# Performance work log

Hardware: AMD Instinct MI355X
Metric: run time of the kernel (lower is better)

Reference implementation:

```python
import jax, jax.numpy as jnp
import numpy as np

N = 50000        # nodes
E = 1_600_000    # edges
F = 32           # in/out channels
T = 4            # towers
FT = F // T      # per-tower channels = 8
ED = 16          # edge_dim
L = 5            # num PNA layers


def setup_inputs() -> dict:
    key = jax.random.key(0)
    ks = jax.random.split(key, 11)
    s = 0.2  # weight scale
    return {
        "x": jax.random.normal(ks[0], (N, F), jnp.float32),
        "edge_index": jax.random.randint(ks[1], (2, E), 0, N, dtype=jnp.int32),
        "edge_attr": jax.random.normal(ks[2], (E, ED), jnp.float32),
        # per-layer stacked PNAConv parameters
        "edge_W": jax.random.normal(ks[3], (L, ED, FT), jnp.float32) * s,
        "edge_b": jax.random.normal(ks[4], (L, FT), jnp.float32) * s,
        "pre_W": jax.random.normal(ks[5], (L, T, 3 * FT, FT), jnp.float32) * s,
        "pre_b": jax.random.normal(ks[6], (L, T, FT), jnp.float32) * s,
        "post_W": jax.random.normal(ks[7], (L, T, 4 * FT, FT), jnp.float32) * s,
        "post_b": jax.random.normal(ks[8], (L, T, FT), jnp.float32) * s,
        "lin_W": jax.random.normal(ks[9], (L, T * FT, F), jnp.float32) * s,
        "lin_b": jax.random.normal(ks[10], (L, F), jnp.float32) * s,
    }


def _pna_layer(x, src, dst, edge_attr, eW, eb, pW, pb, poW, pob, lW, lb):
    n = x.shape[0]
    xt = x.reshape(n, T, FT)                       # divide_input=True
    ee = edge_attr @ eW + eb                       # [E, FT], shared edge encoder
    xi = xt[dst]                                   # target node features [E, T, FT]
    xj = xt[src]                                   # source node features [E, T, FT]
    ee_b = jnp.broadcast_to(ee[:, None, :], (ee.shape[0], T, FT))
    h = jnp.concatenate([xi, xj, ee_b], axis=-1)   # [E, T, 3*FT]
    # per-tower pre-MLP (pre_layers=1)
    h = jnp.einsum('etk,tkf->etf', h, pW) + pb     # [E, T, FT]
    # aggregators: mean, sum, max (scaler = identity)
    ssum = jax.ops.segment_sum(h, dst, num_segments=n)
    cnt = jax.ops.segment_sum(jnp.ones((h.shape[0],), h.dtype), dst, num_segments=n)
    mean = ssum / jnp.maximum(cnt, 1.0)[:, None, None]
    mx = jax.ops.segment_max(h, dst, num_segments=n)
    mx = jnp.where(cnt[:, None, None] > 0, mx, 0.0)  # empty segments -> 0 (PyG convention)
    out = jnp.concatenate([xt, mean, ssum, mx], axis=-1)  # [N, T, 4*FT]
    # per-tower post-MLP (post_layers=1)
    out = jnp.einsum('ntk,tkf->ntf', out, poW) + pob      # [N, T, FT]
    out = out.reshape(n, T * FT) @ lW + lb                # final mixing linear
    return jax.nn.relu(out)


def reference(x, edge_index, edge_attr, edge_W, edge_b, pre_W, pre_b,
              post_W, post_b, lin_W, lin_b):
    src, dst = edge_index[0], edge_index[1]
    for l in range(L):
        x = _pna_layer(x, src, dst, edge_attr,
                       edge_W[l], edge_b[l], pre_W[l], pre_b[l],
                       post_W[l], post_b[l], lin_W[l], lin_b[l])
    return x
```

## Files before the change

kernel.cpp:

```cpp
#include <hip/hip_runtime.h>
#include <hip/hip_fp16.h>

#define NN 50000
#define NE 1600000
#define F 32
#define T 4
#define FT 8
#define ED 16
#define NLAYERS 5


__global__ void zero_cnt(int* __restrict__ cnt) {
    int i = blockIdx.x * 256 + threadIdx.x;
    if (i < NN) cnt[i] = 0;
}

__global__ void count_kernel(const int* __restrict__ ei, int* __restrict__ cnt) {
    int e = blockIdx.x * 256 + threadIdx.x;
    if (e >= NE) return;
    atomicAdd(&cnt[ei[NE + e]], 1);
}

__global__ void scan_kernel(const int* __restrict__ cnt, int* __restrict__ row_ptr,
                            int* __restrict__ cursor) {
    __shared__ int wsum[16];
    __shared__ int carry_s;
    int tid = threadIdx.x;
    int lane = tid & 63, wid = tid >> 6;
    if (tid == 0) carry_s = 0;
    __syncthreads();
    for (int base = 0; base < NN; base += 1024) {
        int i = base + tid;
        int v = (i < NN) ? cnt[i] : 0;
        int s = v;
#pragma unroll
        for (int off = 1; off < 64; off <<= 1) {
            int tt = __shfl_up(s, off, 64);
            if (lane >= off) s += tt;
        }
        __syncthreads();
        if (lane == 63) wsum[wid] = s;
        __syncthreads();
        if (wid == 0 && lane < 16) {
            int w = wsum[lane];
            int ws = w;
#pragma unroll
            for (int off = 1; off < 16; off <<= 1) {
                int tt = __shfl_up(ws, off, 16);
                if (lane >= off) ws += tt;
            }
            wsum[lane] = ws - w;
        }
        __syncthreads();
        int excl = carry_s + wsum[wid] + s - v;
        if (i < NN) { row_ptr[i] = excl; cursor[i] = excl; }
        __syncthreads();
        if (tid == 1023) carry_s += wsum[15] + s;
    }
}

__global__ void build_kernel(const int* __restrict__ ei,
                             const float* __restrict__ eattr,
                             const float* __restrict__ edge_W,
                             const float* __restrict__ edge_b,
                             int* __restrict__ cursor,
                             int* __restrict__ src_s,
                             float4* __restrict__ ee_pm) {
    __shared__ float sW[NLAYERS * ED * FT];
    __shared__ float sB[NLAYERS * FT];
    int tid = threadIdx.x;
    for (int k = tid; k < NLAYERS * ED * FT; k += 256) sW[k] = edge_W[k];
    for (int k = tid; k < NLAYERS * FT; k += 256) sB[k] = edge_b[k];
    __syncthreads();
    int e = blockIdx.x * 256 + tid;
    if (e >= NE) return;
    int src = ei[e];
    int dst = ei[NE + e];
    float ea[16];
    const float4* eap = (const float4*)(eattr + (size_t)e * ED);
#pragma unroll
    for (int q = 0; q < 4; q++) {
        float4 v = eap[q];
        ea[q * 4 + 0] = v.x; ea[q * 4 + 1] = v.y;
        ea[q * 4 + 2] = v.z; ea[q * 4 + 3] = v.w;
    }
    int p = atomicAdd(&cursor[dst], 1);
    src_s[p] = src;
#pragma unroll
    for (int l = 0; l < NLAYERS; l++) {
        float v[8];
#pragma unroll
        for (int j = 0; j < 8; j++) v[j] = sB[l * 8 + j];
#pragma unroll
        for (int k = 0; k < 16; k++) {
            float av = ea[k];
#pragma unroll
            for (int j = 0; j < 8; j++) v[j] += av * sW[l * 128 + k * 8 + j];
        }
        union { __half h[8]; float4 f4; } u;
#pragma unroll
        for (int j = 0; j < 8; j++) u.h[j] = __float2half(v[j]);
        ee_pm[(size_t)l * NE + p] = u.f4;
    }
}


__device__ __forceinline__ unsigned short f2bf_rne(float v) {
    unsigned u = __float_as_uint(v);
    return (unsigned short)((u + 0x7FFFu + ((u >> 16) & 1u)) >> 16);
}

__global__ void node_pre(const float* __restrict__ xin,
                         const float* __restrict__ preW,
                         unsigned short* __restrict__ b16) {
    int idx = blockIdx.x * 256 + threadIdx.x;
    if (idx >= NN * F) return;
    int n = idx >> 5, ch = idx & 31;
    int t = ch >> 3, f = ch & 7;
    const float* xrow = xin + n * F + t * FT;
    const float* wB = preW + (t * 24 + 8) * 8 + f;
    float bv = 0.f;
#pragma unroll
    for (int k = 0; k < 8; k++) bv += xrow[k] * wB[k * 8];
    b16[idx] = f2bf_rne(bv);
}

__global__ __launch_bounds__(256) void gather_post(
        const float* __restrict__ xin,
        const unsigned short* __restrict__ b16,
        const float4* __restrict__ eeL,
        const int* __restrict__ row_ptr, const int* __restrict__ cnt,
        const int* __restrict__ src_s,
        const float* __restrict__ preW,
        const float* __restrict__ preb,
        const float* __restrict__ postW, const float* __restrict__ postb,
        const float* __restrict__ linW, const float* __restrict__ linb,
        float* __restrict__ xout) {
    int tid = threadIdx.x;
    int wv = tid >> 6;
    int lane = tid & 63;
    int ch = lane & 31, half = lane >> 5;
    int n = blockIdx.x * 4 + wv;
    int t = ch >> 3, f = ch & 7;

    float wc8[8];
#pragma unroll
    for (int j = 0; j < 8; j++) wc8[j] = preW[(t * 24 + 16 + j) * 8 + f];

    int rs = row_ptr[n], deg = cnt[n];
    int re = rs + deg;
    float S = 0.f, M = -3.4e38f;
    int i0 = rs + half;

    int s2 = 0;
    float4 e0 = {0,0,0,0}, e1 = {0,0,0,0}, e2 = {0,0,0,0};
    unsigned short b0 = 0, b1 = 0;
    if (i0 < re)     { int s0 = src_s[i0];     e0 = eeL[i0];     b0 = b16[s0 * F + ch]; }
    if (i0 + 2 < re) { int s1 = src_s[i0 + 2]; e1 = eeL[i0 + 2]; b1 = b16[s1 * F + ch]; }
    if (i0 + 4 < re) { s2 = src_s[i0 + 4];     e2 = eeL[i0 + 4]; }

    for (int i = i0; i < re; i += 2) {
        int s3 = s2; float4 e3 = e2; unsigned short b2 = b1;
        if (i + 6 < re) { s3 = src_s[i + 6]; e3 = eeL[i + 6]; }
        if (i + 4 < re) { b2 = b16[s2 * F + ch]; }
        union { float4 f4; __half2 h2[4]; } u; u.f4 = e0;
        float h = __uint_as_float((unsigned)b0 << 16);
#pragma unroll
        for (int q = 0; q < 4; q++) {
            float2 p2 = __half22float2(u.h2[q]);
            h += p2.x * wc8[2 * q] + p2.y * wc8[2 * q + 1];
        }
        S += h;
        M = fmaxf(M, h);
        e0 = e1; e1 = e2; e2 = e3;
        b0 = b1; b1 = b2;
        s2 = s3;
    }
    S += __shfl_xor(S, 32, 64);
    M = fmaxf(M, __shfl_xor(M, 32, 64));

    float xv = xin[(size_t)n * F + ch];
    float a_val = preb[t * 8 + f];
#pragma unroll
    for (int j = 0; j < 8; j++)
        a_val += __shfl(xv, t * 8 + j, 64) * preW[(t * 24 + j) * 8 + f];

    float sum_h, mean_h, max_h;
    if (deg > 0) {
        sum_h = S + (float)deg * a_val;
        mean_h = sum_h / (float)deg;
        max_h = M + a_val;
    } else {
        sum_h = 0.f; mean_h = 0.f; max_h = 0.f;
    }

    float u2 = postb[t * 8 + f];
#pragma unroll
    for (int kk = 0; kk < 8; kk++) {
        int sl = t * 8 + kk;
        u2 += __shfl(xv,     sl, 64) * postW[(t * 32 + 0 * 8 + kk) * 8 + f];
        u2 += __shfl(mean_h, sl, 64) * postW[(t * 32 + 1 * 8 + kk) * 8 + f];
        u2 += __shfl(sum_h,  sl, 64) * postW[(t * 32 + 2 * 8 + kk) * 8 + f];
        u2 += __shfl(max_h,  sl, 64) * postW[(t * 32 + 3 * 8 + kk) * 8 + f];
    }
    float y = linb[ch];
#pragma unroll
    for (int k = 0; k < 32; k++)
        y += __shfl(u2, k, 64) * linW[k * 32 + ch];
    if (half == 0)
        xout[(size_t)n * F + ch] = fmaxf(y, 0.f);
}


extern "C" void kernel_launch(void* const* d_in, const int* in_sizes, int n_in,
                              void* d_out, int out_size, void* d_ws, size_t ws_size,
                              hipStream_t stream) {
    const float* x      = (const float*)d_in[0];
    const int*   ei     = (const int*)d_in[1];
    const float* eattr  = (const float*)d_in[2];
    const float* edge_W = (const float*)d_in[3];
    const float* edge_b = (const float*)d_in[4];
    const float* pre_W  = (const float*)d_in[5];
    const float* pre_b  = (const float*)d_in[6];
    const float* post_W = (const float*)d_in[7];
    const float* post_b = (const float*)d_in[8];
    const float* lin_W  = (const float*)d_in[9];
    const float* lin_b  = (const float*)d_in[10];
    float* out = (float*)d_out;

    const size_t NC = (size_t)NN * F;
    char* p = (char*)d_ws;
    float4* ee_pm = (float4*)p;        p += sizeof(float4) * (size_t)NLAYERS * NE;
    int* src_s    = (int*)p;           p += sizeof(int) * NE;
    int* cnt      = (int*)p;           p += sizeof(int) * NN;
    int* row_ptr  = (int*)p;           p += sizeof(int) * NN;
    int* cursor   = (int*)p;           p += sizeof(int) * NN;
    unsigned short* b16 = (unsigned short*)p;  p += sizeof(unsigned short) * NC;
    float* xb0    = (float*)p;         p += sizeof(float) * NC;
    float* xb1    = (float*)p;         p += sizeof(float) * NC;

    dim3 blk(256);
    int gN  = (NN + 255) / 256;
    int gE  = (NE + 255) / 256;
    int gNC = (NN * F + 255) / 256;
    int gG  = NN / 4;

    hipLaunchKernelGGL(zero_cnt,     dim3(gN), blk, 0, stream, cnt);
    hipLaunchKernelGGL(count_kernel, dim3(gE), blk, 0, stream, ei, cnt);
    hipLaunchKernelGGL(scan_kernel,  dim3(1), dim3(1024), 0, stream, cnt, row_ptr, cursor);
    hipLaunchKernelGGL(build_kernel, dim3(gE), blk, 0, stream, ei, eattr,
                       edge_W, edge_b, cursor, src_s, ee_pm);

    const float* xin = x;
    for (int l = 0; l < NLAYERS; l++) {
        const float* pW  = pre_W  + (size_t)l * T * 24 * FT;
        const float* pb  = pre_b  + (size_t)l * T * FT;
        const float* poW = post_W + (size_t)l * T * 32 * FT;
        const float* pob = post_b + (size_t)l * T * FT;
        const float* lW  = lin_W  + (size_t)l * F * F;
        const float* lb  = lin_b  + (size_t)l * F;
        float* xout = (l == NLAYERS - 1) ? out : ((l & 1) ? xb1 : xb0);

        hipLaunchKernelGGL(node_pre, dim3(gNC), blk, 0, stream, xin, pW, b16);
        hipLaunchKernelGGL(gather_post, dim3(gG), blk, 0, stream,
                           xin, b16, ee_pm + (size_t)l * NE,
                           row_ptr, cnt, src_s, pW, pb,
                           poW, pob, lW, lb, xout);
        xin = xout;
    }
}
```

Baseline: 787.5 us.

## Fold edge encoder into pre-MLP weights and store raw fp16 edge attributes once

```diff
diff --git a/kernel.cpp b/kernel.cpp
--- a/kernel.cpp
+++ b/kernel.cpp
@@ -61,47 +61,28 @@
 
 __global__ void build_kernel(const int* __restrict__ ei,
                              const float* __restrict__ eattr,
-                             const float* __restrict__ edge_W,
-                             const float* __restrict__ edge_b,
                              int* __restrict__ cursor,
                              int* __restrict__ src_s,
-                             float4* __restrict__ ee_pm) {
-    __shared__ float sW[NLAYERS * ED * FT];
-    __shared__ float sB[NLAYERS * FT];
-    int tid = threadIdx.x;
-    for (int k = tid; k < NLAYERS * ED * FT; k += 256) sW[k] = edge_W[k];
-    for (int k = tid; k < NLAYERS * FT; k += 256) sB[k] = edge_b[k];
-    __syncthreads();
-    int e = blockIdx.x * 256 + tid;
+                             float4* __restrict__ eh) {
+    int e = blockIdx.x * 256 + threadIdx.x;
     if (e >= NE) return;
     int src = ei[e];
     int dst = ei[NE + e];
-    float ea[16];
     const float4* eap = (const float4*)(eattr + (size_t)e * ED);
-#pragma unroll
-    for (int q = 0; q < 4; q++) {
-        float4 v = eap[q];
-        ea[q * 4 + 0] = v.x; ea[q * 4 + 1] = v.y;
-        ea[q * 4 + 2] = v.z; ea[q * 4 + 3] = v.w;
-    }
+    float4 v0 = eap[0], v1 = eap[1], v2 = eap[2], v3 = eap[3];
+    union { __half h[16]; float4 f4[2]; } u;
+    u.h[0]  = __float2half(v0.x); u.h[1]  = __float2half(v0.y);
+    u.h[2]  = __float2half(v0.z); u.h[3]  = __float2half(v0.w);
+    u.h[4]  = __float2half(v1.x); u.h[5]  = __float2half(v1.y);
+    u.h[6]  = __float2half(v1.z); u.h[7]  = __float2half(v1.w);
+    u.h[8]  = __float2half(v2.x); u.h[9]  = __float2half(v2.y);
+    u.h[10] = __float2half(v2.z); u.h[11] = __float2half(v2.w);
+    u.h[12] = __float2half(v3.x); u.h[13] = __float2half(v3.y);
+    u.h[14] = __float2half(v3.z); u.h[15] = __float2half(v3.w);
     int p = atomicAdd(&cursor[dst], 1);
     src_s[p] = src;
-#pragma unroll
-    for (int l = 0; l < NLAYERS; l++) {
-        float v[8];
-#pragma unroll
-        for (int j = 0; j < 8; j++) v[j] = sB[l * 8 + j];
-#pragma unroll
-        for (int k = 0; k < 16; k++) {
-            float av = ea[k];
-#pragma unroll
-            for (int j = 0; j < 8; j++) v[j] += av * sW[l * 128 + k * 8 + j];
-        }
-        union { __half h[8]; float4 f4; } u;
-#pragma unroll
-        for (int j = 0; j < 8; j++) u.h[j] = __float2half(v[j]);
-        ee_pm[(size_t)l * NE + p] = u.f4;
-    }
+    eh[2 * (size_t)p]     = u.f4[0];
+    eh[2 * (size_t)p + 1] = u.f4[1];
 }
 
 
@@ -127,14 +108,18 @@
 
 __global__ __launch_bounds__(256) void gather_post(
         const float* __restrict__ xin,
-        const unsigned short* __restrict__ b16,
-        const float4* __restrict__ eeL,
+        const unsigned short* __restrict__ b16_in,
+        unsigned short* __restrict__ b16_out,
+        const float4* __restrict__ eh,
         const int* __restrict__ row_ptr, const int* __restrict__ cnt,
         const int* __restrict__ src_s,
+        const float* __restrict__ eW,
+        const float* __restrict__ ebias,
         const float* __restrict__ preW,
         const float* __restrict__ preb,
         const float* __restrict__ postW, const float* __restrict__ postb,
         const float* __restrict__ linW, const float* __restrict__ linb,
+        const float* __restrict__ preW_next,
         float* __restrict__ xout) {
     int tid = threadIdx.x;
     int wv = tid >> 6;
@@ -143,9 +128,20 @@
     int n = blockIdx.x * 4 + wv;
     int t = ch >> 3, f = ch & 7;
 
-    float wc8[8];
-#pragma unroll
-    for (int j = 0; j < 8; j++) wc8[j] = preW[(t * 24 + 16 + j) * 8 + f];
+    float pj[8];
+#pragma unroll
+    for (int j = 0; j < 8; j++) pj[j] = preW[(t * 24 + 16 + j) * 8 + f];
+    float wc16[16];
+#pragma unroll
+    for (int k = 0; k < 16; k++) {
+        float s = 0.f;
+#pragma unroll
+        for (int j = 0; j < 8; j++) s += eW[k * 8 + j] * pj[j];
+        wc16[k] = s;
+    }
+    float c0 = 0.f;
+#pragma unroll
+    for (int j = 0; j < 8; j++) c0 += ebias[j] * pj[j];
 
     int rs = row_ptr[n], deg = cnt[n];
     int re = rs + deg;
@@ -153,26 +149,40 @@
     int i0 = rs + half;
 
     int s2 = 0;
-    float4 e0 = {0,0,0,0}, e1 = {0,0,0,0}, e2 = {0,0,0,0};
+    float4 l0 = {0,0,0,0}, h0 = {0,0,0,0};
+    float4 l1 = {0,0,0,0}, h1 = {0,0,0,0};
+    float4 l2 = {0,0,0,0}, h2 = {0,0,0,0};
     unsigned short b0 = 0, b1 = 0;
-    if (i0 < re)     { int s0 = src_s[i0];     e0 = eeL[i0];     b0 = b16[s0 * F + ch]; }
-    if (i0 + 2 < re) { int s1 = src_s[i0 + 2]; e1 = eeL[i0 + 2]; b1 = b16[s1 * F + ch]; }
-    if (i0 + 4 < re) { s2 = src_s[i0 + 4];     e2 = eeL[i0 + 4]; }
+    if (i0 < re)     { int s0 = src_s[i0];
+                       l0 = eh[2*(size_t)i0];     h0 = eh[2*(size_t)i0+1];
+                       b0 = b16_in[s0 * F + ch]; }
+    if (i0 + 2 < re) { int s1 = src_s[i0 + 2];
+                       l1 = eh[2*(size_t)(i0+2)]; h1 = eh[2*(size_t)(i0+2)+1];
+                       b1 = b16_in[s1 * F + ch]; }
+    if (i0 + 4 < re) { s2 = src_s[i0 + 4];
+                       l2 = eh[2*(size_t)(i0+4)]; h2 = eh[2*(size_t)(i0+4)+1]; }
 
     for (int i = i0; i < re; i += 2) {
-        int s3 = s2; float4 e3 = e2; unsigned short b2 = b1;
-        if (i + 6 < re) { s3 = src_s[i + 6]; e3 = eeL[i + 6]; }
-        if (i + 4 < re) { b2 = b16[s2 * F + ch]; }
-        union { float4 f4; __half2 h2[4]; } u; u.f4 = e0;
+        int s3 = s2; float4 l3 = l2, h3 = h2; unsigned short b2 = b1;
+        if (i + 6 < re) { s3 = src_s[i + 6];
+                          l3 = eh[2*(size_t)(i+6)]; h3 = eh[2*(size_t)(i+6)+1]; }
+        if (i + 4 < re) { b2 = b16_in[s2 * F + ch]; }
+        union { float4 f4; __half2 hh[4]; } ua, ub;
+        ua.f4 = l0; ub.f4 = h0;
         float h = __uint_as_float((unsigned)b0 << 16);
 #pragma unroll
         for (int q = 0; q < 4; q++) {
-            float2 p2 = __half22float2(u.h2[q]);
-            h += p2.x * wc8[2 * q] + p2.y * wc8[2 * q + 1];
+            float2 pa = __half22float2(ua.hh[q]);
+            h += pa.x * wc16[2 * q] + pa.y * wc16[2 * q + 1];
+        }
+#pragma unroll
+        for (int q = 0; q < 4; q++) {
+            float2 pb = __half22float2(ub.hh[q]);
+            h += pb.x * wc16[8 + 2 * q] + pb.y * wc16[8 + 2 * q + 1];
         }
         S += h;
         M = fmaxf(M, h);
-        e0 = e1; e1 = e2; e2 = e3;
+        l0 = l1; h0 = h1; l1 = l2; h1 = h2; l2 = l3; h2 = h3;
         b0 = b1; b1 = b2;
         s2 = s3;
     }
@@ -180,7 +190,7 @@
     M = fmaxf(M, __shfl_xor(M, 32, 64));
 
     float xv = xin[(size_t)n * F + ch];
-    float a_val = preb[t * 8 + f];
+    float a_val = preb[t * 8 + f] + c0;
 #pragma unroll
     for (int j = 0; j < 8; j++)
         a_val += __shfl(xv, t * 8 + j, 64) * preW[(t * 24 + j) * 8 + f];
@@ -207,8 +217,18 @@
 #pragma unroll
     for (int k = 0; k < 32; k++)
         y += __shfl(u2, k, 64) * linW[k * 32 + ch];
+    y = fmaxf(y, 0.f);
     if (half == 0)
-        xout[(size_t)n * F + ch] = fmaxf(y, 0.f);
+        xout[(size_t)n * F + ch] = y;
+
+    if (preW_next) {
+        float bn = 0.f;
+#pragma unroll
+        for (int j = 0; j < 8; j++)
+            bn += __shfl(y, t * 8 + j, 64) * preW_next[(t * 24 + 8 + j) * 8 + f];
+        if (half == 0)
+            b16_out[(size_t)n * F + ch] = f2bf_rne(bn);
+    }
 }
 
 
@@ -230,12 +250,13 @@
 
     const size_t NC = (size_t)NN * F;
     char* p = (char*)d_ws;
-    float4* ee_pm = (float4*)p;        p += sizeof(float4) * (size_t)NLAYERS * NE;
+    float4* eh    = (float4*)p;        p += sizeof(float4) * 2 * (size_t)NE;
     int* src_s    = (int*)p;           p += sizeof(int) * NE;
     int* cnt      = (int*)p;           p += sizeof(int) * NN;
     int* row_ptr  = (int*)p;           p += sizeof(int) * NN;
     int* cursor   = (int*)p;           p += sizeof(int) * NN;
-    unsigned short* b16 = (unsigned short*)p;  p += sizeof(unsigned short) * NC;
+    unsigned short* b16a = (unsigned short*)p;  p += sizeof(unsigned short) * NC;
+    unsigned short* b16b = (unsigned short*)p;  p += sizeof(unsigned short) * NC;
     float* xb0    = (float*)p;         p += sizeof(float) * NC;
     float* xb1    = (float*)p;         p += sizeof(float) * NC;
 
@@ -249,23 +270,29 @@
     hipLaunchKernelGGL(count_kernel, dim3(gE), blk, 0, stream, ei, cnt);
     hipLaunchKernelGGL(scan_kernel,  dim3(1), dim3(1024), 0, stream, cnt, row_ptr, cursor);
     hipLaunchKernelGGL(build_kernel, dim3(gE), blk, 0, stream, ei, eattr,
-                       edge_W, edge_b, cursor, src_s, ee_pm);
+                       cursor, src_s, eh);
+
+    hipLaunchKernelGGL(node_pre, dim3(gNC), blk, 0, stream, x, pre_W, b16a);
 
     const float* xin = x;
     for (int l = 0; l < NLAYERS; l++) {
+        const float* eWl = edge_W + (size_t)l * ED * FT;
+        const float* ebl = edge_b + (size_t)l * FT;
         const float* pW  = pre_W  + (size_t)l * T * 24 * FT;
         const float* pb  = pre_b  + (size_t)l * T * FT;
         const float* poW = post_W + (size_t)l * T * 32 * FT;
         const float* pob = post_b + (size_t)l * T * FT;
         const float* lW  = lin_W  + (size_t)l * F * F;
         const float* lb  = lin_b  + (size_t)l * F;
+        const float* pWn = (l + 1 < NLAYERS) ? (pre_W + (size_t)(l + 1) * T * 24 * FT)
+                                             : nullptr;
         float* xout = (l == NLAYERS - 1) ? out : ((l & 1) ? xb1 : xb0);
-
-        hipLaunchKernelGGL(node_pre, dim3(gNC), blk, 0, stream, xin, pW, b16);
+        const unsigned short* bin  = (l & 1) ? b16b : b16a;
+        unsigned short*       bout = (l & 1) ? b16a : b16b;
+
         hipLaunchKernelGGL(gather_post, dim3(gG), blk, 0, stream,
-                           xin, b16, ee_pm + (size_t)l * NE,
-                           row_ptr, cnt, src_s, pW, pb,
-                           poW, pob, lW, lb, xout);
+                           xin, bin, pWn ? bout : nullptr, eh, row_ptr, cnt, src_s,
+                           eWl, ebl, pW, pb, poW, pob, lW, lb, pWn, xout);
         xin = xout;
     }
 }
```

After: 876.2 us. 11.3% more time.
